# Optimization experiments

Hardware: AMD Instinct MI355X
Metric: run time of the kernel (lower is better)

Reference implementation:

```python
import jax, jax.numpy as jnp
import numpy as np
from jax import lax

B, T, D, U = 64, 512, 512, 1024


def setup_inputs() -> dict:
    key = jax.random.key(0)
    k1, k2, k3 = jax.random.split(key, 3)
    x = jax.random.normal(k1, (B, T, D), dtype=jnp.float32)
    Wx = jax.random.normal(k2, (D, 4 * U), dtype=jnp.float32) * (1.0 / np.sqrt(D))
    Wh = jax.random.normal(k3, (U, 4 * U), dtype=jnp.float32) * (1.0 / np.sqrt(U))
    # bias init: zeros(i), ones(f), zeros(c), zeros(o)
    b = jnp.concatenate([jnp.zeros((U,)), jnp.ones((U,)), jnp.zeros((2 * U,))]).astype(jnp.float32)
    return {"x": x, "Wx": Wx, "Wh": Wh, "b": b}


def reference(x, Wx, Wh, b):
    units = Wh.shape[0]
    batch = x.shape[0]
    # Precompute input projections for all timesteps: [B, T, 4U]
    xz = jnp.einsum('btd,dz->btz', x, Wx)

    def step(carry, zx_t):
        h, c = carry
        z = zx_t + h @ Wh + b            # [B, 4U]
        zi, zf, zg, zo = jnp.split(z, 4, axis=-1)
        i = jax.nn.sigmoid(zi)
        f = jax.nn.sigmoid(zf)
        c_new = f * c + i * jnp.tanh(zg)
        o = jax.nn.sigmoid(zo)
        h_new = o * jnp.tanh(c_new)
        return (h_new, c_new), None

    h0 = jnp.zeros((batch, units), dtype=x.dtype)
    c0 = jnp.zeros((batch, units), dtype=x.dtype)
    (h_last, c_last), _ = lax.scan(step, (h0, c0), jnp.swapaxes(xz, 0, 1))
    # return_sequence=False, return_states=False -> last hidden state
    return h_last
```

## Files before the change

### kernel.cpp

```cpp
#include <hip/hip_runtime.h>
#include <hip/hip_bf16.h>


#define T_STEPS 512
#define BATCH   64
#define DIM     512
#define UNITS   1024
#define ZCOLS   4096
#define MR      16

typedef float        f32x4 __attribute__((ext_vector_type(4)));
typedef unsigned int u32x4 __attribute__((ext_vector_type(4)));

__device__ __forceinline__ f32x4 mfma16x16x32_bf16(u32x4 a, u32x4 b, f32x4 c) {
    asm("v_mfma_f32_16x16x32_bf16 %0, %1, %2, %0" : "+v"(c) : "v"(a), "v"(b));
    return c;
}

__device__ __forceinline__ unsigned short f2bf(float f) {
    union { float f; unsigned u; } v; v.f = f;
    unsigned r = v.u + 0x7fffu + ((v.u >> 16) & 1u);
    return (unsigned short)(r >> 16);
}

__device__ __forceinline__ float fsigmoid(float x) { return 1.0f / (1.0f + __expf(-x)); }
__device__ __forceinline__ float ftanh(float x)    { return 1.0f - 2.0f / (__expf(2.0f * x) + 1.0f); }

__device__ __forceinline__ u32x4 pack8(const float* __restrict__ p) {
    float4 f0 = reinterpret_cast<const float4*>(p)[0];
    float4 f1 = reinterpret_cast<const float4*>(p)[1];
    u32x4 r;
    r.x = (unsigned)f2bf(f0.x) | ((unsigned)f2bf(f0.y) << 16);
    r.y = (unsigned)f2bf(f0.z) | ((unsigned)f2bf(f0.w) << 16);
    r.z = (unsigned)f2bf(f1.x) | ((unsigned)f2bf(f1.y) << 16);
    r.w = (unsigned)f2bf(f1.z) | ((unsigned)f2bf(f1.w) << 16);
    return r;
}

#define LD4(d, base) \
    asm volatile("global_load_dwordx4 %0, %1, off sc0 sc1" : "=v"(d) : "v"(base));
#define WAITV0 \
    asm volatile("s_waitcnt vmcnt(0)" ::: "memory"); \
    __builtin_amdgcn_sched_barrier(0);


__global__ void k_transpose_bf16(const float* __restrict__ in, unsigned short* __restrict__ out,
                                 int K, int N) {
    __shared__ float tile[32][33];
    int n0 = blockIdx.x * 32, k0 = blockIdx.y * 32;
    int tx = threadIdx.x, ty = threadIdx.y;
    tile[ty][tx] = in[(size_t)(k0 + ty) * N + n0 + tx];
    __syncthreads();
    out[(size_t)(n0 + ty) * K + k0 + tx] = f2bf(tile[tx][ty]);
}

__global__ void k_init(unsigned int* __restrict__ hbuf_u32, float* __restrict__ cbuf,
                       unsigned int* __restrict__ flags) {
    int i = blockIdx.x * blockDim.x + threadIdx.x;
    if (i < 65536) hbuf_u32[i] = 0u;
    else if (i < 131072) cbuf[i - 65536] = 0.0f;
    else if (i < 131072 + 4096) flags[i - 131072] = 0u;
}

__global__ __launch_bounds__(512, 2) void k_xproj(
        const float* __restrict__ x,
        const unsigned short* __restrict__ WxT,
        const float* __restrict__ bias,
        float* __restrict__ xz,
        int base) {
    const int tid  = threadIdx.x;
    const int lane = tid & 63;
    const int w    = tid >> 6;
    const int n0   = blockIdx.x * 512 + w * 64;
    const int t    = blockIdx.y;
    const int r16  = lane & 15;
    const int kl   = (lane >> 4) * 8;

    __shared__ __align__(16) unsigned short as_[64 * 512];

    for (int i = tid; i < 4096; i += 512) {
        int row = i >> 6, kc = i & 63;
        u32x4 v = pack8(x + ((size_t)row * T_STEPS + base + t) * DIM + kc * 8);
        int lb = (row * 1024 + kc * 16) ^ ((row & 7) << 4);
        *reinterpret_cast<u32x4*>(reinterpret_cast<char*>(as_) + lb) = v;
    }
    __syncthreads();

    const unsigned short* bp = WxT + (size_t)(n0 + r16) * DIM + kl;

    f32x4 acc[4][4] = {};
    asm volatile("s_nop 1" : "+v"(acc[0][0]), "+v"(acc[1][1]), "+v"(acc[2][2]), "+v"(acc[3][3]));

    #pragma unroll 2
    for (int kk = 0; kk < 16; ++kk) {
        u32x4 b0 = *reinterpret_cast<const u32x4*>(bp + kk * 32);
        u32x4 b1 = *reinterpret_cast<const u32x4*>(bp + 16 * DIM + kk * 32);
        u32x4 b2 = *reinterpret_cast<const u32x4*>(bp + 32 * DIM + kk * 32);
        u32x4 b3 = *reinterpret_cast<const u32x4*>(bp + 48 * DIM + kk * 32);
        u32x4 a[4];
        #pragma unroll
        for (int mt = 0; mt < 4; ++mt) {
            int row = mt * 16 + r16;
            int lb = (row * 1024 + (kk * 32 + kl) * 2) ^ ((row & 7) << 4);
            a[mt] = *reinterpret_cast<const u32x4*>(reinterpret_cast<const char*>(as_) + lb);
        }
        #pragma unroll
        for (int mt = 0; mt < 4; ++mt) {
            acc[mt][0] = mfma16x16x32_bf16(a[mt], b0, acc[mt][0]);
            acc[mt][1] = mfma16x16x32_bf16(a[mt], b1, acc[mt][1]);
            acc[mt][2] = mfma16x16x32_bf16(a[mt], b2, acc[mt][2]);
            acc[mt][3] = mfma16x16x32_bf16(a[mt], b3, acc[mt][3]);
        }
    }
    asm volatile("s_nop 7\n\ts_nop 7" : "+v"(acc[0][0]), "+v"(acc[1][1]), "+v"(acc[2][2]), "+v"(acc[3][3]));

    const int rowq = (lane >> 4) * 4;
    #pragma unroll
    for (int nt = 0; nt < 4; ++nt) {
        const int col = n0 + nt * 16 + r16;
        const float bv = bias[col];
        #pragma unroll
        for (int mt = 0; mt < 4; ++mt)
            #pragma unroll
            for (int r = 0; r < 4; ++r)
                xz[((size_t)t * BATCH + mt * 16 + rowq + r) * ZCOLS + col] = acc[mt][nt][r] + bv;
    }
}

__global__ __launch_bounds__(512, 1) void k_lstm(
        const float* __restrict__ xz,
        const unsigned short* __restrict__ WhT,
        unsigned short* hbuf,
        float* __restrict__ cbuf,
        float* __restrict__ out,
        unsigned int* flags,
        int base_step, int tc) {
    const int tid  = threadIdx.x;
    const int lane = tid & 63;
    const int w    = tid >> 6;
    const int ct   = w & 3;
    const int kh   = w >> 2;
    const int mg   = blockIdx.x >> 5;
    const int zb   = blockIdx.x & 31;
    const int r0   = mg * MR;
    const int u0   = zb * 32;
    const int c16  = lane & 15;
    const int klb  = (lane >> 4) * 16;

    __shared__ __align__(16) unsigned short hs[MR * 1024];
    __shared__ float zbuf[2][MR][132];

    u32x4 breg[2][16];
    #pragma unroll
    for (int n = 0; n < 2; ++n) {
        const unsigned short* wp =
            WhT + ((size_t)(ct * UNITS + u0 + n * 16 + c16)) * UNITS + kh * 512 + (lane >> 4) * 8;
        #pragma unroll
        for (int kk = 0; kk < 16; ++kk) {
            breg[n][kk] = *reinterpret_cast<const u32x4*>(wp + kk * 32);
            asm volatile("" : "+v"(breg[n][kk]));
        }
    }

    const int ri = tid >> 5;
    const int ui = tid & 31;
    float creg = cbuf[(size_t)(r0 + ri) * UNITS + u0 + ui];

    unsigned int* const myflag = flags + (size_t)blockIdx.x * 32;
    const unsigned int* const gflags = flags + (size_t)mg * 32 * 32;

    for (int t = 0; t < tc; ++t) {
        const int s = base_step + t;
        const unsigned short* hrd = hbuf + (size_t)(s & 1) * (BATCH * UNITS);

        {
            u32x4 sv[4];
            #pragma unroll
            for (int j = 0; j < 4; ++j) {
                int i = tid + j * 512;
                int row = i >> 7, kc = i & 127;
                const unsigned short* src = hrd + (size_t)(r0 + row) * UNITS + kc * 8;
                LD4(sv[j], src)
            }
            WAITV0
            #pragma unroll
            for (int j = 0; j < 4; ++j) {
                int i = tid + j * 512;
                int row = i >> 7, kc = i & 127;
                int lb = (row * 2048 + kc * 16) ^ ((row & 7) << 4);
                *reinterpret_cast<u32x4*>(reinterpret_cast<char*>(hs) + lb) = sv[j];
            }
        }
        __syncthreads();

        const float* xp = xz + ((size_t)t * BATCH + r0 + ri) * ZCOLS + u0 + ui;
        float xv0 = xp[0], xv1 = xp[UNITS], xv2 = xp[2 * UNITS], xv3 = xp[3 * UNITS];

        f32x4 acc0 = {0, 0, 0, 0}, acc1 = {0, 0, 0, 0};
        asm volatile("s_nop 1" : "+v"(acc0), "+v"(acc1));
        const char* abase = reinterpret_cast<const char*>(hs);
        const int axor = (c16 & 7) << 4;
        #pragma unroll
        for (int kk = 0; kk < 16; ++kk) {
            int lb = (c16 * 2048 + kh * 1024 + kk * 64 + klb) ^ axor;
            u32x4 a = *reinterpret_cast<const u32x4*>(abase + lb);
            acc0 = mfma16x16x32_bf16(a, breg[0][kk], acc0);
            acc1 = mfma16x16x32_bf16(a, breg[1][kk], acc1);
        }
        asm volatile("s_nop 7\n\ts_nop 7" : "+v"(acc0), "+v"(acc1));
        {
            const int rowq = (lane >> 4) * 4;
            #pragma unroll
            for (int r = 0; r < 4; ++r) {
                zbuf[kh][rowq + r][ct * 32 + c16]      = acc0[r];
                zbuf[kh][rowq + r][ct * 32 + 16 + c16] = acc1[r];
            }
        }
        __syncthreads();

        {
            float zi = zbuf[0][ri][ui]      + zbuf[1][ri][ui]      + xv0;
            float zf = zbuf[0][ri][32 + ui] + zbuf[1][ri][32 + ui] + xv1;
            float zg = zbuf[0][ri][64 + ui] + zbuf[1][ri][64 + ui] + xv2;
            float zo = zbuf[0][ri][96 + ui] + zbuf[1][ri][96 + ui] + xv3;
            float ig = fsigmoid(zi), fg = fsigmoid(zf), gg = ftanh(zg), og = fsigmoid(zo);
            creg = fg * creg + ig * gg;
            float hn = og * ftanh(creg);
            unsigned hv = f2bf(hn);
            unsigned short* hwp = hbuf + (size_t)((s + 1) & 1) * (BATCH * UNITS)
                                  + (size_t)(r0 + ri) * UNITS + u0 + ui;
            asm volatile("global_store_short %0, %1, off sc0 sc1" :: "v"(hwp), "v"(hv) : "memory");
            if (s == T_STEPS - 1) out[(size_t)(r0 + ri) * UNITS + u0 + ui] = hn;
        }

        if (t < tc - 1) {
            WAITV0
            __syncthreads();
            if (tid == 0) {
                unsigned fv = (unsigned)(s + 1);
                asm volatile("global_store_dword %0, %1, off sc0 sc1"
                             :: "v"(myflag), "v"(fv) : "memory");
                asm volatile("s_waitcnt vmcnt(0)" ::: "memory");
            }
            if (w == 0) {
                const unsigned tgt = (unsigned)(s + 1);
                const unsigned int* fp = gflags + (size_t)(lane & 31) * 32;
                int iter = 0;
                for (;;) {
                    unsigned v;
                    asm volatile("global_load_dword %0, %1, off sc0 sc1\n\ts_waitcnt vmcnt(0)"
                                 : "=v"(v) : "v"(fp) : "memory");
                    if (__all((int)(v >= tgt))) break;
                    if (++iter > (1 << 20)) break;
                    __builtin_amdgcn_s_sleep(1);
                }
            }
            __syncthreads();
        }
    }
    cbuf[(size_t)(r0 + ri) * UNITS + u0 + ui] = creg;
}


extern "C" void kernel_launch(void* const* d_in, const int* in_sizes, int n_in,
                              void* d_out, int out_size, void* d_ws, size_t ws_size,
                              hipStream_t stream) {
    const float* x    = (const float*)d_in[0];
    const float* Wx   = (const float*)d_in[1];
    const float* Wh   = (const float*)d_in[2];
    const float* bias = (const float*)d_in[3];

    char* ws = (char*)d_ws;
    unsigned short* WxT   = (unsigned short*)(ws);
    unsigned short* WhT   = (unsigned short*)(ws + (4u << 20));
    unsigned short* hbuf  = (unsigned short*)(ws + (12u << 20));
    float*          cbuf  = (float*)(ws + (12u << 20) + (256u << 10));
    unsigned int*   flags = (unsigned int*)(ws + (12u << 20) + (512u << 10));
    float*          xz    = (float*)(ws + (13u << 20));

    const size_t fixedB = 13u << 20;
    int tc = 1;
    const int cands[9] = {512, 256, 128, 64, 32, 16, 8, 4, 2};
    for (int i = 0; i < 9; ++i)
        if (fixedB + (size_t)cands[i] * (1u << 20) <= ws_size) { tc = cands[i]; break; }

    k_transpose_bf16<<<dim3(128, 16), dim3(32, 32), 0, stream>>>(Wx, WxT, 512, 4096);
    k_transpose_bf16<<<dim3(128, 32), dim3(32, 32), 0, stream>>>(Wh, WhT, 1024, 4096);
    k_init<<<512, 512, 0, stream>>>((unsigned int*)hbuf, cbuf, flags);

    const int nch = T_STEPS / tc;
    for (int ci = 0; ci < nch; ++ci) {
        k_xproj<<<dim3(8, tc), 512, 0, stream>>>(x, WxT, bias, xz, ci * tc);
        k_lstm<<<128, 512, 0, stream>>>(xz, WhT, hbuf, cbuf, (float*)d_out, flags,
                                        ci * tc, tc);
    }
}
```

Baseline: 1.905 ms.

## Replace flag barrier with step-tagged hidden-state polling and double the LSTM blocks

The per-step cross-block flag barrier is removed. Each hidden value is now stored as a 32-bit word holding the step index in its upper half and the bf16 value in its lower half, and consumers poll the h rows they need until every tag matches the current step. The LSTM grid goes from 128 to 256 blocks, with 8 batch rows per block instead of 16, so only half the threads do the elementwise gate math. This is meant to cut barrier latency and let each block wait only on the data it reads, at the cost of doubling h traffic and repeating the recurrent weight loads across more blocks. The MFMA A-tile rows beyond 8 now alias via c16&7, so half of the MFMA output is redundant.

After: 2.579 ms. 35.4% more time.

```diff
diff --git a/kernel.cpp b/kernel.cpp
--- a/kernel.cpp
+++ b/kernel.cpp
@@ -7,7 +7,6 @@
 #define DIM     512
 #define UNITS   1024
 #define ZCOLS   4096
-#define MR      16
 
 typedef float        f32x4 __attribute__((ext_vector_type(4)));
 typedef unsigned int u32x4 __attribute__((ext_vector_type(4)));
@@ -37,8 +36,8 @@
     return r;
 }
 
-#define LD4(d, base) \
-    asm volatile("global_load_dwordx4 %0, %1, off sc0 sc1" : "=v"(d) : "v"(base));
+#define LDX4T(d, p) \
+    asm volatile("global_load_dwordx4 %0, %1, off sc0 sc1" : "=v"(d) : "v"(p));
 #define WAITV0 \
     asm volatile("s_waitcnt vmcnt(0)" ::: "memory"); \
     __builtin_amdgcn_sched_barrier(0);
@@ -54,12 +53,10 @@
     out[(size_t)(n0 + ty) * K + k0 + tx] = f2bf(tile[tx][ty]);
 }
 
-__global__ void k_init(unsigned int* __restrict__ hbuf_u32, float* __restrict__ cbuf,
-                       unsigned int* __restrict__ flags) {
+__global__ void k_init(unsigned int* __restrict__ hbuf_u32, float* __restrict__ cbuf) {
     int i = blockIdx.x * blockDim.x + threadIdx.x;
-    if (i < 65536) hbuf_u32[i] = 0u;
-    else if (i < 131072) cbuf[i - 65536] = 0.0f;
-    else if (i < 131072 + 4096) flags[i - 131072] = 0u;
+    if (i < 131072) hbuf_u32[i] = 0u;
+    else if (i < 196608) cbuf[i - 131072] = 0.0f;
 }
 
 __global__ __launch_bounds__(512, 2) void k_xproj(
@@ -130,25 +127,24 @@
 __global__ __launch_bounds__(512, 1) void k_lstm(
         const float* __restrict__ xz,
         const unsigned short* __restrict__ WhT,
-        unsigned short* hbuf,
+        unsigned int* hbuf,
         float* __restrict__ cbuf,
         float* __restrict__ out,
-        unsigned int* flags,
         int base_step, int tc) {
     const int tid  = threadIdx.x;
     const int lane = tid & 63;
     const int w    = tid >> 6;
     const int ct   = w & 3;
     const int kh   = w >> 2;
-    const int mg   = blockIdx.x >> 5;
-    const int zb   = blockIdx.x & 31;
-    const int r0   = mg * MR;
-    const int u0   = zb * 32;
+    const int grp  = blockIdx.x & 7;
+    const int zs   = blockIdx.x >> 3;
+    const int r0   = grp * 8;
+    const int u0   = zs * 32;
     const int c16  = lane & 15;
     const int klb  = (lane >> 4) * 16;
 
-    __shared__ __align__(16) unsigned short hs[MR * 1024];
-    __shared__ float zbuf[2][MR][132];
+    __shared__ __align__(16) unsigned short hs[8 * 1024];
+    __shared__ float zb[32 * 132];
 
     u32x4 breg[2][16];
     #pragma unroll
@@ -164,46 +160,66 @@
 
     const int ri = tid >> 5;
     const int ui = tid & 31;
-    float creg = cbuf[(size_t)(r0 + ri) * UNITS + u0 + ui];
-
-    unsigned int* const myflag = flags + (size_t)blockIdx.x * 32;
-    const unsigned int* const gflags = flags + (size_t)mg * 32 * 32;
+    float creg = 0.0f;
+    if (tid < 256) creg = cbuf[(size_t)(r0 + ri) * UNITS + u0 + ui];
+
+    const int srow  = tid >> 6;
+    const int scol0 = (tid & 63) * 16;
+    const int sbase = srow * 2048 + scol0 * 2;
+    const int sxor  = (srow & 7) << 4;
 
     for (int t = 0; t < tc; ++t) {
         const int s = base_step + t;
-        const unsigned short* hrd = hbuf + (size_t)(s & 1) * (BATCH * UNITS);
 
         {
-            u32x4 sv[4];
-            #pragma unroll
-            for (int j = 0; j < 4; ++j) {
-                int i = tid + j * 512;
-                int row = i >> 7, kc = i & 127;
-                const unsigned short* src = hrd + (size_t)(r0 + row) * UNITS + kc * 8;
-                LD4(sv[j], src)
+            const unsigned int* sp = hbuf + (size_t)(s & 1) * (BATCH * UNITS)
+                                     + (size_t)(r0 + srow) * UNITS + scol0;
+            const unsigned want = (unsigned)s;
+            u32x4 v0, v1, v2, v3;
+            int iter = 0;
+            for (;;) {
+                LDX4T(v0, sp) LDX4T(v1, sp + 4) LDX4T(v2, sp + 8) LDX4T(v3, sp + 12)
+                WAITV0
+                bool ok = ((v0.x >> 16) == want) & ((v0.y >> 16) == want) &
+                          ((v0.z >> 16) == want) & ((v0.w >> 16) == want) &
+                          ((v1.x >> 16) == want) & ((v1.y >> 16) == want) &
+                          ((v1.z >> 16) == want) & ((v1.w >> 16) == want) &
+                          ((v2.x >> 16) == want) & ((v2.y >> 16) == want) &
+                          ((v2.z >> 16) == want) & ((v2.w >> 16) == want) &
+                          ((v3.x >> 16) == want) & ((v3.y >> 16) == want) &
+                          ((v3.z >> 16) == want) & ((v3.w >> 16) == want);
+                if (ok) break;
+                if (++iter > (1 << 16)) break;
+                __builtin_amdgcn_s_sleep(1);
             }
-            WAITV0
-            #pragma unroll
-            for (int j = 0; j < 4; ++j) {
-                int i = tid + j * 512;
-                int row = i >> 7, kc = i & 127;
-                int lb = (row * 2048 + kc * 16) ^ ((row & 7) << 4);
-                *reinterpret_cast<u32x4*>(reinterpret_cast<char*>(hs) + lb) = sv[j];
-            }
+            u32x4 A, B;
+            A.x = (v0.x & 0xffffu) | (v0.y << 16);
+            A.y = (v0.z & 0xffffu) | (v0.w << 16);
+            A.z = (v1.x & 0xffffu) | (v1.y << 16);
+            A.w = (v1.z & 0xffffu) | (v1.w << 16);
+            B.x = (v2.x & 0xffffu) | (v2.y << 16);
+            B.y = (v2.z & 0xffffu) | (v2.w << 16);
+            B.z = (v3.x & 0xffffu) | (v3.y << 16);
+            B.w = (v3.z & 0xffffu) | (v3.w << 16);
+            *reinterpret_cast<u32x4*>(reinterpret_cast<char*>(hs) + (sbase ^ sxor))        = A;
+            *reinterpret_cast<u32x4*>(reinterpret_cast<char*>(hs) + ((sbase + 16) ^ sxor)) = B;
         }
         __syncthreads();
 
-        const float* xp = xz + ((size_t)t * BATCH + r0 + ri) * ZCOLS + u0 + ui;
-        float xv0 = xp[0], xv1 = xp[UNITS], xv2 = xp[2 * UNITS], xv3 = xp[3 * UNITS];
+        float xv0 = 0, xv1 = 0, xv2 = 0, xv3 = 0;
+        if (tid < 256) {
+            const float* xp = xz + ((size_t)t * BATCH + r0 + ri) * ZCOLS + u0 + ui;
+            xv0 = xp[0]; xv1 = xp[UNITS]; xv2 = xp[2 * UNITS]; xv3 = xp[3 * UNITS];
+        }
 
         f32x4 acc0 = {0, 0, 0, 0}, acc1 = {0, 0, 0, 0};
         asm volatile("s_nop 1" : "+v"(acc0), "+v"(acc1));
         const char* abase = reinterpret_cast<const char*>(hs);
         const int axor = (c16 & 7) << 4;
+        const int aoff = (c16 & 7) * 2048 + kh * 1024 + klb;
         #pragma unroll
         for (int kk = 0; kk < 16; ++kk) {
-            int lb = (c16 * 2048 + kh * 1024 + kk * 64 + klb) ^ axor;
-            u32x4 a = *reinterpret_cast<const u32x4*>(abase + lb);
+            u32x4 a = *reinterpret_cast<const u32x4*>(abase + ((aoff + kk * 64) ^ axor));
             acc0 = mfma16x16x32_bf16(a, breg[0][kk], acc0);
             acc1 = mfma16x16x32_bf16(a, breg[1][kk], acc1);
         }
@@ -212,53 +228,28 @@
             const int rowq = (lane >> 4) * 4;
             #pragma unroll
             for (int r = 0; r < 4; ++r) {
-                zbuf[kh][rowq + r][ct * 32 + c16]      = acc0[r];
-                zbuf[kh][rowq + r][ct * 32 + 16 + c16] = acc1[r];
+                zb[(kh * 16 + rowq + r) * 132 + ct * 32 + c16]      = acc0[r];
+                zb[(kh * 16 + rowq + r) * 132 + ct * 32 + 16 + c16] = acc1[r];
             }
         }
         __syncthreads();
 
-        {
-            float zi = zbuf[0][ri][ui]      + zbuf[1][ri][ui]      + xv0;
-            float zf = zbuf[0][ri][32 + ui] + zbuf[1][ri][32 + ui] + xv1;
-            float zg = zbuf[0][ri][64 + ui] + zbuf[1][ri][64 + ui] + xv2;
-            float zo = zbuf[0][ri][96 + ui] + zbuf[1][ri][96 + ui] + xv3;
+        if (tid < 256) {
+            float zi = zb[ri * 132 + ui]      + zb[(16 + ri) * 132 + ui]      + xv0;
+            float zf = zb[ri * 132 + 32 + ui] + zb[(16 + ri) * 132 + 32 + ui] + xv1;
+            float zg = zb[ri * 132 + 64 + ui] + zb[(16 + ri) * 132 + 64 + ui] + xv2;
+            float zo = zb[ri * 132 + 96 + ui] + zb[(16 + ri) * 132 + 96 + ui] + xv3;
             float ig = fsigmoid(zi), fg = fsigmoid(zf), gg = ftanh(zg), og = fsigmoid(zo);
             creg = fg * creg + ig * gg;
             float hn = og * ftanh(creg);
-            unsigned hv = f2bf(hn);
-            unsigned short* hwp = hbuf + (size_t)((s + 1) & 1) * (BATCH * UNITS)
-                                  + (size_t)(r0 + ri) * UNITS + u0 + ui;
-            asm volatile("global_store_short %0, %1, off sc0 sc1" :: "v"(hwp), "v"(hv) : "memory");
+            unsigned hv = ((unsigned)(s + 1) << 16) | (unsigned)f2bf(hn);
+            unsigned int* hwp = hbuf + (size_t)((s + 1) & 1) * (BATCH * UNITS)
+                                + (size_t)(r0 + ri) * UNITS + u0 + ui;
+            asm volatile("global_store_dword %0, %1, off sc0 sc1" :: "v"(hwp), "v"(hv) : "memory");
             if (s == T_STEPS - 1) out[(size_t)(r0 + ri) * UNITS + u0 + ui] = hn;
         }
-
-        if (t < tc - 1) {
-            WAITV0
-            __syncthreads();
-            if (tid == 0) {
-                unsigned fv = (unsigned)(s + 1);
-                asm volatile("global_store_dword %0, %1, off sc0 sc1"
-                             :: "v"(myflag), "v"(fv) : "memory");
-                asm volatile("s_waitcnt vmcnt(0)" ::: "memory");
-            }
-            if (w == 0) {
-                const unsigned tgt = (unsigned)(s + 1);
-                const unsigned int* fp = gflags + (size_t)(lane & 31) * 32;
-                int iter = 0;
-                for (;;) {
-                    unsigned v;
-                    asm volatile("global_load_dword %0, %1, off sc0 sc1\n\ts_waitcnt vmcnt(0)"
-                                 : "=v"(v) : "v"(fp) : "memory");
-                    if (__all((int)(v >= tgt))) break;
-                    if (++iter > (1 << 20)) break;
-                    __builtin_amdgcn_s_sleep(1);
-                }
-            }
-            __syncthreads();
-        }
-    }
-    cbuf[(size_t)(r0 + ri) * UNITS + u0 + ui] = creg;
+    }
+    if (tid < 256) cbuf[(size_t)(r0 + ri) * UNITS + u0 + ui] = creg;
 }
 
 
@@ -273,9 +264,8 @@
     char* ws = (char*)d_ws;
     unsigned short* WxT   = (unsigned short*)(ws);
     unsigned short* WhT   = (unsigned short*)(ws + (4u << 20));
-    unsigned short* hbuf  = (unsigned short*)(ws + (12u << 20));
-    float*          cbuf  = (float*)(ws + (12u << 20) + (256u << 10));
-    unsigned int*   flags = (unsigned int*)(ws + (12u << 20) + (512u << 10));
+    unsigned int*   hbuf  = (unsigned int*)(ws + (12u << 20));
+    float*          cbuf  = (float*)(ws + (12u << 20) + (512u << 10));
     float*          xz    = (float*)(ws + (13u << 20));
 
     const size_t fixedB = 13u << 20;
@@ -286,12 +276,12 @@
 
     k_transpose_bf16<<<dim3(128, 16), dim3(32, 32), 0, stream>>>(Wx, WxT, 512, 4096);
     k_transpose_bf16<<<dim3(128, 32), dim3(32, 32), 0, stream>>>(Wh, WhT, 1024, 4096);
-    k_init<<<512, 512, 0, stream>>>((unsigned int*)hbuf, cbuf, flags);
+    k_init<<<512, 512, 0, stream>>>(hbuf, cbuf);
 
     const int nch = T_STEPS / tc;
     for (int ci = 0; ci < nch; ++ci) {
         k_xproj<<<dim3(8, tc), 512, 0, stream>>>(x, WxT, bias, xz, ci * tc);
-        k_lstm<<<128, 512, 0, stream>>>(xz, WhT, hbuf, cbuf, (float*)d_out, flags,
+        k_lstm<<<256, 512, 0, stream>>>(xz, WhT, hbuf, cbuf, (float*)d_out,
                                         ci * tc, tc);
     }
 }
```

## Fuse input projection into persistent LSTM kernel, compute next step during barrier wait

Applied to the files above, without the earlier changes.

Removes the separate xproj kernel and its global xz buffer. Each persistent LSTM block now computes its own slice of x_t·Wx with MFMA, using a small shared x tile and a double-buffered xzb array. The projection for step s+1 runs after the block publishes its flag and before it spins on the other blocks' flags, so the work is meant to hide inside the grid-wide sync wait. This drops the global round trip of the projection output and the chunked multi-launch structure. In exchange each step reloads Wx fragments from global or L2, and the spin-wait iteration cap is lowered.

Result: slower. 3.660 ms (+92.1%).

```diff
diff --git a/kernel.cpp b/kernel.cpp
--- a/kernel.cpp
+++ b/kernel.cpp
@@ -54,87 +54,20 @@
     out[(size_t)(n0 + ty) * K + k0 + tx] = f2bf(tile[tx][ty]);
 }
 
-__global__ void k_init(unsigned int* __restrict__ hbuf_u32, float* __restrict__ cbuf,
-                       unsigned int* __restrict__ flags) {
+__global__ void k_init(unsigned int* __restrict__ hbuf_u32, unsigned int* __restrict__ flags) {
     int i = blockIdx.x * blockDim.x + threadIdx.x;
     if (i < 65536) hbuf_u32[i] = 0u;
-    else if (i < 131072) cbuf[i - 65536] = 0.0f;
-    else if (i < 131072 + 4096) flags[i - 131072] = 0u;
-}
-
-__global__ __launch_bounds__(512, 2) void k_xproj(
+    else if (i < 65536 + 4096) flags[i - 65536] = 0u;
+}
+
+__global__ __launch_bounds__(512, 1) void k_lstm(
         const float* __restrict__ x,
         const unsigned short* __restrict__ WxT,
+        const unsigned short* __restrict__ WhT,
         const float* __restrict__ bias,
-        float* __restrict__ xz,
-        int base) {
-    const int tid  = threadIdx.x;
-    const int lane = tid & 63;
-    const int w    = tid >> 6;
-    const int n0   = blockIdx.x * 512 + w * 64;
-    const int t    = blockIdx.y;
-    const int r16  = lane & 15;
-    const int kl   = (lane >> 4) * 8;
-
-    __shared__ __align__(16) unsigned short as_[64 * 512];
-
-    for (int i = tid; i < 4096; i += 512) {
-        int row = i >> 6, kc = i & 63;
-        u32x4 v = pack8(x + ((size_t)row * T_STEPS + base + t) * DIM + kc * 8);
-        int lb = (row * 1024 + kc * 16) ^ ((row & 7) << 4);
-        *reinterpret_cast<u32x4*>(reinterpret_cast<char*>(as_) + lb) = v;
-    }
-    __syncthreads();
-
-    const unsigned short* bp = WxT + (size_t)(n0 + r16) * DIM + kl;
-
-    f32x4 acc[4][4] = {};
-    asm volatile("s_nop 1" : "+v"(acc[0][0]), "+v"(acc[1][1]), "+v"(acc[2][2]), "+v"(acc[3][3]));
-
-    #pragma unroll 2
-    for (int kk = 0; kk < 16; ++kk) {
-        u32x4 b0 = *reinterpret_cast<const u32x4*>(bp + kk * 32);
-        u32x4 b1 = *reinterpret_cast<const u32x4*>(bp + 16 * DIM + kk * 32);
-        u32x4 b2 = *reinterpret_cast<const u32x4*>(bp + 32 * DIM + kk * 32);
-        u32x4 b3 = *reinterpret_cast<const u32x4*>(bp + 48 * DIM + kk * 32);
-        u32x4 a[4];
-        #pragma unroll
-        for (int mt = 0; mt < 4; ++mt) {
-            int row = mt * 16 + r16;
-            int lb = (row * 1024 + (kk * 32 + kl) * 2) ^ ((row & 7) << 4);
-            a[mt] = *reinterpret_cast<const u32x4*>(reinterpret_cast<const char*>(as_) + lb);
-        }
-        #pragma unroll
-        for (int mt = 0; mt < 4; ++mt) {
-            acc[mt][0] = mfma16x16x32_bf16(a[mt], b0, acc[mt][0]);
-            acc[mt][1] = mfma16x16x32_bf16(a[mt], b1, acc[mt][1]);
-            acc[mt][2] = mfma16x16x32_bf16(a[mt], b2, acc[mt][2]);
-            acc[mt][3] = mfma16x16x32_bf16(a[mt], b3, acc[mt][3]);
-        }
-    }
-    asm volatile("s_nop 7\n\ts_nop 7" : "+v"(acc[0][0]), "+v"(acc[1][1]), "+v"(acc[2][2]), "+v"(acc[3][3]));
-
-    const int rowq = (lane >> 4) * 4;
-    #pragma unroll
-    for (int nt = 0; nt < 4; ++nt) {
-        const int col = n0 + nt * 16 + r16;
-        const float bv = bias[col];
-        #pragma unroll
-        for (int mt = 0; mt < 4; ++mt)
-            #pragma unroll
-            for (int r = 0; r < 4; ++r)
-                xz[((size_t)t * BATCH + mt * 16 + rowq + r) * ZCOLS + col] = acc[mt][nt][r] + bv;
-    }
-}
-
-__global__ __launch_bounds__(512, 1) void k_lstm(
-        const float* __restrict__ xz,
-        const unsigned short* __restrict__ WhT,
         unsigned short* hbuf,
-        float* __restrict__ cbuf,
         float* __restrict__ out,
-        unsigned int* flags,
-        int base_step, int tc) {
+        unsigned int* flags) {
     const int tid  = threadIdx.x;
     const int lane = tid & 63;
     const int w    = tid >> 6;
@@ -145,16 +78,19 @@
     const int r0   = mg * MR;
     const int u0   = zb * 32;
     const int c16  = lane & 15;
+    const int kl   = (lane >> 4) * 8;
     const int klb  = (lane >> 4) * 16;
 
     __shared__ __align__(16) unsigned short hs[MR * 1024];
     __shared__ float zbuf[2][MR][132];
+    __shared__ __align__(16) unsigned short xs[MR * 512];
+    __shared__ float xzb[2][MR][132];
 
     u32x4 breg[2][16];
     #pragma unroll
     for (int n = 0; n < 2; ++n) {
         const unsigned short* wp =
-            WhT + ((size_t)(ct * UNITS + u0 + n * 16 + c16)) * UNITS + kh * 512 + (lane >> 4) * 8;
+            WhT + ((size_t)(ct * UNITS + u0 + n * 16 + c16)) * UNITS + kh * 512 + kl;
         #pragma unroll
         for (int kk = 0; kk < 16; ++kk) {
             breg[n][kk] = *reinterpret_cast<const u32x4*>(wp + kk * 32);
@@ -164,13 +100,47 @@
 
     const int ri = tid >> 5;
     const int ui = tid & 31;
-    float creg = cbuf[(size_t)(r0 + ri) * UNITS + u0 + ui];
+    float creg = 0.0f;
+    float bi0 = bias[u0 + ui];
+    float bi1 = bias[UNITS + u0 + ui];
+    float bi2 = bias[2 * UNITS + u0 + ui];
+    float bi3 = bias[3 * UNITS + u0 + ui];
 
     unsigned int* const myflag = flags + (size_t)blockIdx.x * 32;
     const unsigned int* const gflags = flags + (size_t)mg * 32 * 32;
 
-    for (int t = 0; t < tc; ++t) {
-        const int s = base_step + t;
+    const unsigned short* const bpx =
+        WxT + ((size_t)((w >> 1) * UNITS + u0 + (w & 1) * 16 + c16)) * DIM + kl;
+
+
+    {
+        #pragma unroll
+        for (int j = 0; j < 2; ++j) {
+            int i = tid + j * 512;
+            int row = i >> 6, kc8 = i & 63;
+            u32x4 v = pack8(x + ((size_t)(r0 + row) * T_STEPS + 0) * DIM + kc8 * 8);
+            int lb = (row * 1024 + kc8 * 16) ^ ((row & 7) << 4);
+            *reinterpret_cast<u32x4*>(reinterpret_cast<char*>(xs) + lb) = v;
+        }
+        __syncthreads();
+        f32x4 xacc = {0, 0, 0, 0};
+        asm volatile("s_nop 1" : "+v"(xacc));
+        #pragma unroll
+        for (int kk = 0; kk < 16; ++kk) {
+            u32x4 b = *reinterpret_cast<const u32x4*>(bpx + kk * 32);
+            int lb = (c16 * 1024 + (kk * 32 + kl) * 2) ^ ((c16 & 7) << 4);
+            u32x4 a = *reinterpret_cast<const u32x4*>(reinterpret_cast<const char*>(xs) + lb);
+            xacc = mfma16x16x32_bf16(a, b, xacc);
+        }
+        asm volatile("s_nop 7\n\ts_nop 7" : "+v"(xacc));
+        const int rowq = (lane >> 4) * 4;
+        #pragma unroll
+        for (int r = 0; r < 4; ++r)
+            xzb[0][rowq + r][w * 16 + c16] = xacc[r];
+        __syncthreads();
+    }
+
+    for (int s = 0; s < T_STEPS; ++s) {
         const unsigned short* hrd = hbuf + (size_t)(s & 1) * (BATCH * UNITS);
 
         {
@@ -193,9 +163,6 @@
         }
         __syncthreads();
 
-        const float* xp = xz + ((size_t)t * BATCH + r0 + ri) * ZCOLS + u0 + ui;
-        float xv0 = xp[0], xv1 = xp[UNITS], xv2 = xp[2 * UNITS], xv3 = xp[3 * UNITS];
-
         f32x4 acc0 = {0, 0, 0, 0}, acc1 = {0, 0, 0, 0};
         asm volatile("s_nop 1" : "+v"(acc0), "+v"(acc1));
         const char* abase = reinterpret_cast<const char*>(hs);
@@ -219,10 +186,11 @@
         __syncthreads();
 
         {
-            float zi = zbuf[0][ri][ui]      + zbuf[1][ri][ui]      + xv0;
-            float zf = zbuf[0][ri][32 + ui] + zbuf[1][ri][32 + ui] + xv1;
-            float zg = zbuf[0][ri][64 + ui] + zbuf[1][ri][64 + ui] + xv2;
-            float zo = zbuf[0][ri][96 + ui] + zbuf[1][ri][96 + ui] + xv3;
+            const float* xzr = xzb[s & 1][ri];
+            float zi = zbuf[0][ri][ui]      + zbuf[1][ri][ui]      + xzr[ui]      + bi0;
+            float zf = zbuf[0][ri][32 + ui] + zbuf[1][ri][32 + ui] + xzr[32 + ui] + bi1;
+            float zg = zbuf[0][ri][64 + ui] + zbuf[1][ri][64 + ui] + xzr[64 + ui] + bi2;
+            float zo = zbuf[0][ri][96 + ui] + zbuf[1][ri][96 + ui] + xzr[96 + ui] + bi3;
             float ig = fsigmoid(zi), fg = fsigmoid(zf), gg = ftanh(zg), og = fsigmoid(zo);
             creg = fg * creg + ig * gg;
             float hn = og * ftanh(creg);
@@ -233,7 +201,7 @@
             if (s == T_STEPS - 1) out[(size_t)(r0 + ri) * UNITS + u0 + ui] = hn;
         }
 
-        if (t < tc - 1) {
+        if (s < T_STEPS - 1) {
             WAITV0
             __syncthreads();
             if (tid == 0) {
@@ -242,6 +210,34 @@
                              :: "v"(myflag), "v"(fv) : "memory");
                 asm volatile("s_waitcnt vmcnt(0)" ::: "memory");
             }
+
+            {
+                #pragma unroll
+                for (int j = 0; j < 2; ++j) {
+                    int i = tid + j * 512;
+                    int row = i >> 6, kc8 = i & 63;
+                    u32x4 v = pack8(x + ((size_t)(r0 + row) * T_STEPS + (s + 1)) * DIM + kc8 * 8);
+                    int lb = (row * 1024 + kc8 * 16) ^ ((row & 7) << 4);
+                    *reinterpret_cast<u32x4*>(reinterpret_cast<char*>(xs) + lb) = v;
+                }
+                __syncthreads();
+                f32x4 xacc = {0, 0, 0, 0};
+                asm volatile("s_nop 1" : "+v"(xacc));
+                #pragma unroll
+                for (int kk = 0; kk < 16; ++kk) {
+                    u32x4 b = *reinterpret_cast<const u32x4*>(bpx + kk * 32);
+                    int lb = (c16 * 1024 + (kk * 32 + kl) * 2) ^ ((c16 & 7) << 4);
+                    u32x4 a = *reinterpret_cast<const u32x4*>(reinterpret_cast<const char*>(xs) + lb);
+                    xacc = mfma16x16x32_bf16(a, b, xacc);
+                }
+                asm volatile("s_nop 7\n\ts_nop 7" : "+v"(xacc));
+                const int rowq = (lane >> 4) * 4;
+                #pragma unroll
+                for (int r = 0; r < 4; ++r)
+                    xzb[(s + 1) & 1][rowq + r][w * 16 + c16] = xacc[r];
+            }
+            __syncthreads();
+
             if (w == 0) {
                 const unsigned tgt = (unsigned)(s + 1);
                 const unsigned int* fp = gflags + (size_t)(lane & 31) * 32;
@@ -251,14 +247,13 @@
                     asm volatile("global_load_dword %0, %1, off sc0 sc1\n\ts_waitcnt vmcnt(0)"
                                  : "=v"(v) : "v"(fp) : "memory");
                     if (__all((int)(v >= tgt))) break;
-                    if (++iter > (1 << 20)) break;
+                    if (++iter > (1 << 18)) break;
                     __builtin_amdgcn_s_sleep(1);
                 }
             }
             __syncthreads();
         }
     }
-    cbuf[(size_t)(r0 + ri) * UNITS + u0 + ui] = creg;
 }
 
 
@@ -274,24 +269,11 @@
     unsigned short* WxT   = (unsigned short*)(ws);
     unsigned short* WhT   = (unsigned short*)(ws + (4u << 20));
     unsigned short* hbuf  = (unsigned short*)(ws + (12u << 20));
-    float*          cbuf  = (float*)(ws + (12u << 20) + (256u << 10));
-    unsigned int*   flags = (unsigned int*)(ws + (12u << 20) + (512u << 10));
-    float*          xz    = (float*)(ws + (13u << 20));
-
-    const size_t fixedB = 13u << 20;
-    int tc = 1;
-    const int cands[9] = {512, 256, 128, 64, 32, 16, 8, 4, 2};
-    for (int i = 0; i < 9; ++i)
-        if (fixedB + (size_t)cands[i] * (1u << 20) <= ws_size) { tc = cands[i]; break; }
+    unsigned int*   flags = (unsigned int*)(ws + (12u << 20) + (256u << 10));
 
     k_transpose_bf16<<<dim3(128, 16), dim3(32, 32), 0, stream>>>(Wx, WxT, 512, 4096);
     k_transpose_bf16<<<dim3(128, 32), dim3(32, 32), 0, stream>>>(Wh, WhT, 1024, 4096);
-    k_init<<<512, 512, 0, stream>>>((unsigned int*)hbuf, cbuf, flags);
-
-    const int nch = T_STEPS / tc;
-    for (int ci = 0; ci < nch; ++ci) {
-        k_xproj<<<dim3(8, tc), 512, 0, stream>>>(x, WxT, bias, xz, ci * tc);
-        k_lstm<<<128, 512, 0, stream>>>(xz, WhT, hbuf, cbuf, (float*)d_out, flags,
-                                        ci * tc, tc);
-    }
-}
+    k_init<<<160, 512, 0, stream>>>((unsigned int*)hbuf, flags);
+
+    k_lstm<<<128, 512, 0, stream>>>(x, WxT, WhT, bias, hbuf, (float*)d_out, flags);
+}
```

## Fuse input projection and LSTM recurrence into one persistent producer-consumer kernel

Applied to the files above, without the earlier changes.

Replaces the separate x-projection and recurrent kernels with a single persistent kernel of 256 blocks. 128 blocks run the recurrence and 128 producer blocks compute the input projection into a 64-step ring buffer, coordinated through global flags. This overlaps the input GEMM with the serial recurrence and avoids materializing the full xz tensor and the chunked launches. It relies on all 256 blocks being co-resident and adds spin-wait overhead in the recurrence loop, which now also polls the xz flags each step.

After: 1.643 ms, median of 2. 13.8% less time.

```diff
diff --git a/kernel.cpp b/kernel.cpp
--- a/kernel.cpp
+++ b/kernel.cpp
@@ -8,6 +8,7 @@
 #define UNITS   1024
 #define ZCOLS   4096
 #define MR      16
+#define RING    64
 
 typedef float        f32x4 __attribute__((ext_vector_type(4)));
 typedef unsigned int u32x4 __attribute__((ext_vector_type(4)));
@@ -39,6 +40,11 @@
 
 #define LD4(d, base) \
     asm volatile("global_load_dwordx4 %0, %1, off sc0 sc1" : "=v"(d) : "v"(base));
+#define LDW(d, base) \
+    asm volatile("global_load_dword %0, %1, off sc0 sc1\n\ts_waitcnt vmcnt(0)" \
+                 : "=v"(d) : "v"(base) : "memory");
+#define STW(base, v) \
+    asm volatile("global_store_dword %0, %1, off sc0 sc1" :: "v"(base), "v"(v) : "memory");
 #define WAITV0 \
     asm volatile("s_waitcnt vmcnt(0)" ::: "memory"); \
     __builtin_amdgcn_sched_barrier(0);
@@ -54,211 +60,259 @@
     out[(size_t)(n0 + ty) * K + k0 + tx] = f2bf(tile[tx][ty]);
 }
 
-__global__ void k_init(unsigned int* __restrict__ hbuf_u32, float* __restrict__ cbuf,
-                       unsigned int* __restrict__ flags) {
+__global__ void k_init(unsigned int* __restrict__ hbuf_u32,
+                       unsigned int* __restrict__ hflags,
+                       unsigned int* __restrict__ xzflags) {
     int i = blockIdx.x * blockDim.x + threadIdx.x;
     if (i < 65536) hbuf_u32[i] = 0u;
-    else if (i < 131072) cbuf[i - 65536] = 0.0f;
-    else if (i < 131072 + 4096) flags[i - 131072] = 0u;
-}
-
-__global__ __launch_bounds__(512, 2) void k_xproj(
+    else if (i < 65536 + 4096) hflags[i - 65536] = 0u;
+    else if (i < 65536 + 4096 + 512) xzflags[i - 69632] = 0u;
+}
+
+__global__ __launch_bounds__(512, 1) void k_fused(
         const float* __restrict__ x,
         const unsigned short* __restrict__ WxT,
+        const unsigned short* __restrict__ WhT,
         const float* __restrict__ bias,
-        float* __restrict__ xz,
-        int base) {
+        unsigned short* hbuf,
+        float* __restrict__ out,
+        unsigned int* hflags,
+        unsigned int* xzflags,
+        float* __restrict__ xzring) {
+    __shared__ __align__(16) char smem[65536];
     const int tid  = threadIdx.x;
     const int lane = tid & 63;
     const int w    = tid >> 6;
-    const int n0   = blockIdx.x * 512 + w * 64;
-    const int t    = blockIdx.y;
-    const int r16  = lane & 15;
-    const int kl   = (lane >> 4) * 8;
-
-    __shared__ __align__(16) unsigned short as_[64 * 512];
-
-    for (int i = tid; i < 4096; i += 512) {
-        int row = i >> 6, kc = i & 63;
-        u32x4 v = pack8(x + ((size_t)row * T_STEPS + base + t) * DIM + kc * 8);
-        int lb = (row * 1024 + kc * 16) ^ ((row & 7) << 4);
-        *reinterpret_cast<u32x4*>(reinterpret_cast<char*>(as_) + lb) = v;
-    }
-    __syncthreads();
-
-    const unsigned short* bp = WxT + (size_t)(n0 + r16) * DIM + kl;
-
-    f32x4 acc[4][4] = {};
-    asm volatile("s_nop 1" : "+v"(acc[0][0]), "+v"(acc[1][1]), "+v"(acc[2][2]), "+v"(acc[3][3]));
-
-    #pragma unroll 2
-    for (int kk = 0; kk < 16; ++kk) {
-        u32x4 b0 = *reinterpret_cast<const u32x4*>(bp + kk * 32);
-        u32x4 b1 = *reinterpret_cast<const u32x4*>(bp + 16 * DIM + kk * 32);
-        u32x4 b2 = *reinterpret_cast<const u32x4*>(bp + 32 * DIM + kk * 32);
-        u32x4 b3 = *reinterpret_cast<const u32x4*>(bp + 48 * DIM + kk * 32);
-        u32x4 a[4];
+
+    if (blockIdx.x < 128) {
+        unsigned short* hs = (unsigned short*)smem;
+        float* zb = (float*)(smem + 32768);
+        const int ct  = w & 3;
+        const int kh  = w >> 2;
+        const int mg  = blockIdx.x >> 5;
+        const int zbk = blockIdx.x & 31;
+        const int r0  = mg * MR;
+        const int u0  = zbk * 32;
+        const int c16 = lane & 15;
+        const int kl  = (lane >> 4) * 8;
+        const int klb = (lane >> 4) * 16;
+
+        u32x4 breg[2][16];
         #pragma unroll
-        for (int mt = 0; mt < 4; ++mt) {
-            int row = mt * 16 + r16;
-            int lb = (row * 1024 + (kk * 32 + kl) * 2) ^ ((row & 7) << 4);
-            a[mt] = *reinterpret_cast<const u32x4*>(reinterpret_cast<const char*>(as_) + lb);
+        for (int n = 0; n < 2; ++n) {
+            const unsigned short* wp =
+                WhT + ((size_t)(ct * UNITS + u0 + n * 16 + c16)) * UNITS + kh * 512 + kl;
+            #pragma unroll
+            for (int kk = 0; kk < 16; ++kk) {
+                breg[n][kk] = *reinterpret_cast<const u32x4*>(wp + kk * 32);
+                asm volatile("" : "+v"(breg[n][kk]));
+            }
         }
-        #pragma unroll
-        for (int mt = 0; mt < 4; ++mt) {
-            acc[mt][0] = mfma16x16x32_bf16(a[mt], b0, acc[mt][0]);
-            acc[mt][1] = mfma16x16x32_bf16(a[mt], b1, acc[mt][1]);
-            acc[mt][2] = mfma16x16x32_bf16(a[mt], b2, acc[mt][2]);
-            acc[mt][3] = mfma16x16x32_bf16(a[mt], b3, acc[mt][3]);
+
+        const int ri = tid >> 5;
+        const int ui = tid & 31;
+        float creg = 0.0f;
+
+        unsigned int* const myflag = hflags + (size_t)blockIdx.x * 32;
+        const unsigned int* const gflags = hflags + (size_t)mg * 32 * 32;
+
+        if (w == 0) {
+            const unsigned int* fp = xzflags + (lane & 7);
+            int iter = 0;
+            for (;;) {
+                unsigned v; LDW(v, fp)
+                bool ok = (lane < 8) ? (v == 1u) : true;
+                if (__all((int)ok)) break;
+                if (++iter > (1 << 20)) break;
+                __builtin_amdgcn_s_sleep(1);
+            }
+        }
+        __syncthreads();
+
+        for (int s = 0; s < T_STEPS; ++s) {
+            const unsigned short* hrd = hbuf + (size_t)(s & 1) * (BATCH * UNITS);
+
+            {
+                u32x4 sv[4];
+                #pragma unroll
+                for (int j = 0; j < 4; ++j) {
+                    int i = tid + j * 512;
+                    int row = i >> 7, kc = i & 127;
+                    const unsigned short* src = hrd + (size_t)(r0 + row) * UNITS + kc * 8;
+                    LD4(sv[j], src)
+                }
+                WAITV0
+                #pragma unroll
+                for (int j = 0; j < 4; ++j) {
+                    int i = tid + j * 512;
+                    int row = i >> 7, kc = i & 127;
+                    int lb = (row * 2048 + kc * 16) ^ ((row & 7) << 4);
+                    *reinterpret_cast<u32x4*>(reinterpret_cast<char*>(hs) + lb) = sv[j];
+                }
+            }
+            __syncthreads();
+
+            float xv0, xv1, xv2, xv3;
+            {
+                const float* xp = xzring + ((size_t)(s & (RING - 1)) * BATCH + r0 + ri) * ZCOLS
+                                  + u0 + ui;
+                asm volatile("global_load_dword %0, %1, off sc0 sc1" : "=v"(xv0) : "v"(xp));
+                asm volatile("global_load_dword %0, %1, off sc0 sc1" : "=v"(xv1) : "v"(xp + UNITS));
+                asm volatile("global_load_dword %0, %1, off sc0 sc1" : "=v"(xv2) : "v"(xp + 2 * UNITS));
+                asm volatile("global_load_dword %0, %1, off sc0 sc1" : "=v"(xv3) : "v"(xp + 3 * UNITS));
+            }
+
+            f32x4 acc0 = {0, 0, 0, 0}, acc1 = {0, 0, 0, 0};
+            asm volatile("s_nop 1" : "+v"(acc0), "+v"(acc1));
+            const char* abase = reinterpret_cast<const char*>(hs);
+            const int axor = (c16 & 7) << 4;
+            #pragma unroll
+            for (int kk = 0; kk < 16; ++kk) {
+                int lb = (c16 * 2048 + kh * 1024 + kk * 64 + klb) ^ axor;
+                u32x4 a = *reinterpret_cast<const u32x4*>(abase + lb);
+                acc0 = mfma16x16x32_bf16(a, breg[0][kk], acc0);
+                acc1 = mfma16x16x32_bf16(a, breg[1][kk], acc1);
+            }
+            asm volatile("s_nop 7\n\ts_nop 7" : "+v"(acc0), "+v"(acc1));
+            {
+                const int rowq = (lane >> 4) * 4;
+                #pragma unroll
+                for (int r = 0; r < 4; ++r) {
+                    zb[((kh * 16 + rowq + r)) * 132 + ct * 32 + c16]      = acc0[r];
+                    zb[((kh * 16 + rowq + r)) * 132 + ct * 32 + 16 + c16] = acc1[r];
+                }
+            }
+            __syncthreads();
+            WAITV0
+
+            {
+                float zi = zb[ri * 132 + ui]      + zb[(16 + ri) * 132 + ui]      + xv0;
+                float zf = zb[ri * 132 + 32 + ui] + zb[(16 + ri) * 132 + 32 + ui] + xv1;
+                float zg = zb[ri * 132 + 64 + ui] + zb[(16 + ri) * 132 + 64 + ui] + xv2;
+                float zo = zb[ri * 132 + 96 + ui] + zb[(16 + ri) * 132 + 96 + ui] + xv3;
+                float ig = fsigmoid(zi), fg = fsigmoid(zf), gg = ftanh(zg), og = fsigmoid(zo);
+                creg = fg * creg + ig * gg;
+                float hn = og * ftanh(creg);
+                unsigned hv = f2bf(hn);
+                unsigned short* hwp = hbuf + (size_t)((s + 1) & 1) * (BATCH * UNITS)
+                                      + (size_t)(r0 + ri) * UNITS + u0 + ui;
+                asm volatile("global_store_short %0, %1, off sc0 sc1" :: "v"(hwp), "v"(hv) : "memory");
+                if (s == T_STEPS - 1) out[(size_t)(r0 + ri) * UNITS + u0 + ui] = hn;
+            }
+
+            if (s < T_STEPS - 1) {
+                WAITV0
+                __syncthreads();
+                if (tid == 0) {
+                    STW(myflag, (unsigned)(s + 1))
+                    asm volatile("s_waitcnt vmcnt(0)" ::: "memory");
+                }
+                if (w == 0) {
+                    const unsigned tgtH = (unsigned)(s + 1);
+                    const unsigned tgtX = (unsigned)(s + 2);
+                    const unsigned int* fp = (lane < 32)
+                        ? gflags + (size_t)lane * 32
+                        : xzflags + (size_t)((s + 1) & (RING - 1)) * 8 + (lane & 7);
+                    int iter = 0;
+                    for (;;) {
+                        unsigned v; LDW(v, fp)
+                        bool ok = (lane < 32) ? (v >= tgtH)
+                                  : ((lane < 40) ? (v == tgtX) : true);
+                        if (__all((int)ok)) break;
+                        if (++iter > (1 << 20)) break;
+                        __builtin_amdgcn_s_sleep(1);
+                    }
+                }
+                __syncthreads();
+            }
+        }
+    } else {
+        unsigned short* as_ = (unsigned short*)smem;
+        const int p   = blockIdx.x - 128;
+        const int bx  = p & 7;
+        const int jt  = p >> 3;
+        const int n0  = bx * 512 + w * 64;
+        const int r16 = lane & 15;
+        const int kl  = (lane >> 4) * 8;
+
+        for (int k2 = 0; k2 < T_STEPS / 16; ++k2) {
+            const int t = jt + 16 * k2;
+
+            if (t >= RING) {
+                if (w == 0) {
+                    const unsigned need = (unsigned)(t - RING + 1);
+                    int iter = 0;
+                    for (;;) {
+                        unsigned v0, v1;
+                        LDW(v0, hflags + (size_t)lane * 32)
+                        LDW(v1, hflags + (size_t)(lane + 64) * 32)
+                        if (__all((int)(v0 >= need && v1 >= need))) break;
+                        if (++iter > (1 << 20)) break;
+                        __builtin_amdgcn_s_sleep(1);
+                    }
+                }
+                __syncthreads();
+            }
+
+            for (int i = tid; i < 4096; i += 512) {
+                int row = i >> 6, kc8 = i & 63;
+                u32x4 v = pack8(x + ((size_t)row * T_STEPS + t) * DIM + kc8 * 8);
+                int lb = (row * 1024 + kc8 * 16) ^ ((row & 7) << 4);
+                *reinterpret_cast<u32x4*>(reinterpret_cast<char*>(as_) + lb) = v;
+            }
+            __syncthreads();
+
+            const unsigned short* bp = WxT + (size_t)(n0 + r16) * DIM + kl;
+            f32x4 acc[4][4] = {};
+            asm volatile("s_nop 1" : "+v"(acc[0][0]), "+v"(acc[1][1]), "+v"(acc[2][2]), "+v"(acc[3][3]));
+            #pragma unroll 2
+            for (int kk = 0; kk < 16; ++kk) {
+                u32x4 b0 = *reinterpret_cast<const u32x4*>(bp + kk * 32);
+                u32x4 b1 = *reinterpret_cast<const u32x4*>(bp + 16 * DIM + kk * 32);
+                u32x4 b2 = *reinterpret_cast<const u32x4*>(bp + 32 * DIM + kk * 32);
+                u32x4 b3 = *reinterpret_cast<const u32x4*>(bp + 48 * DIM + kk * 32);
+                u32x4 a[4];
+                #pragma unroll
+                for (int mt = 0; mt < 4; ++mt) {
+                    int row = mt * 16 + r16;
+                    int lb = (row * 1024 + (kk * 32 + kl) * 2) ^ ((row & 7) << 4);
+                    a[mt] = *reinterpret_cast<const u32x4*>(reinterpret_cast<const char*>(as_) + lb);
+                }
+                #pragma unroll
+                for (int mt = 0; mt < 4; ++mt) {
+                    acc[mt][0] = mfma16x16x32_bf16(a[mt], b0, acc[mt][0]);
+                    acc[mt][1] = mfma16x16x32_bf16(a[mt], b1, acc[mt][1]);
+                    acc[mt][2] = mfma16x16x32_bf16(a[mt], b2, acc[mt][2]);
+                    acc[mt][3] = mfma16x16x32_bf16(a[mt], b3, acc[mt][3]);
+                }
+            }
+            asm volatile("s_nop 7\n\ts_nop 7" : "+v"(acc[0][0]), "+v"(acc[1][1]), "+v"(acc[2][2]), "+v"(acc[3][3]));
+
+            {
+                float* ringb = xzring + (size_t)(t & (RING - 1)) * BATCH * ZCOLS;
+                const int rowq = (lane >> 4) * 4;
+                #pragma unroll
+                for (int nt = 0; nt < 4; ++nt) {
+                    const int col = n0 + nt * 16 + r16;
+                    const float bv = bias[col];
+                    #pragma unroll
+                    for (int mt = 0; mt < 4; ++mt) {
+                        #pragma unroll
+                        for (int r = 0; r < 4; ++r) {
+                            float val = acc[mt][nt][r] + bv;
+                            float* dst = ringb + (size_t)(mt * 16 + rowq + r) * ZCOLS + col;
+                            asm volatile("global_store_dword %0, %1, off sc0 sc1"
+                                         :: "v"(dst), "v"(val) : "memory");
+                        }
+                    }
+                }
+            }
+            WAITV0
+            __syncthreads();
+            if (tid == 0) STW(xzflags + (size_t)(t & (RING - 1)) * 8 + bx, (unsigned)(t + 1))
+            __syncthreads();
         }
     }
-    asm volatile("s_nop 7\n\ts_nop 7" : "+v"(acc[0][0]), "+v"(acc[1][1]), "+v"(acc[2][2]), "+v"(acc[3][3]));
-
-    const int rowq = (lane >> 4) * 4;
-    #pragma unroll
-    for (int nt = 0; nt < 4; ++nt) {
-        const int col = n0 + nt * 16 + r16;
-        const float bv = bias[col];
-        #pragma unroll
-        for (int mt = 0; mt < 4; ++mt)
-            #pragma unroll
-            for (int r = 0; r < 4; ++r)
-                xz[((size_t)t * BATCH + mt * 16 + rowq + r) * ZCOLS + col] = acc[mt][nt][r] + bv;
-    }
-}
-
-__global__ __launch_bounds__(512, 1) void k_lstm(
-        const float* __restrict__ xz,
-        const unsigned short* __restrict__ WhT,
-        unsigned short* hbuf,
-        float* __restrict__ cbuf,
-        float* __restrict__ out,
-        unsigned int* flags,
-        int base_step, int tc) {
-    const int tid  = threadIdx.x;
-    const int lane = tid & 63;
-    const int w    = tid >> 6;
-    const int ct   = w & 3;
-    const int kh   = w >> 2;
-    const int mg   = blockIdx.x >> 5;
-    const int zb   = blockIdx.x & 31;
-    const int r0   = mg * MR;
-    const int u0   = zb * 32;
-    const int c16  = lane & 15;
-    const int klb  = (lane >> 4) * 16;
-
-    __shared__ __align__(16) unsigned short hs[MR * 1024];
-    __shared__ float zbuf[2][MR][132];
-
-    u32x4 breg[2][16];
-    #pragma unroll
-    for (int n = 0; n < 2; ++n) {
-        const unsigned short* wp =
-            WhT + ((size_t)(ct * UNITS + u0 + n * 16 + c16)) * UNITS + kh * 512 + (lane >> 4) * 8;
-        #pragma unroll
-        for (int kk = 0; kk < 16; ++kk) {
-            breg[n][kk] = *reinterpret_cast<const u32x4*>(wp + kk * 32);
-            asm volatile("" : "+v"(breg[n][kk]));
-        }
-    }
-
-    const int ri = tid >> 5;
-    const int ui = tid & 31;
-    float creg = cbuf[(size_t)(r0 + ri) * UNITS + u0 + ui];
-
-    unsigned int* const myflag = flags + (size_t)blockIdx.x * 32;
-    const unsigned int* const gflags = flags + (size_t)mg * 32 * 32;
-
-    for (int t = 0; t < tc; ++t) {
-        const int s = base_step + t;
-        const unsigned short* hrd = hbuf + (size_t)(s & 1) * (BATCH * UNITS);
-
-        {
-            u32x4 sv[4];
-            #pragma unroll
-            for (int j = 0; j < 4; ++j) {
-                int i = tid + j * 512;
-                int row = i >> 7, kc = i & 127;
-                const unsigned short* src = hrd + (size_t)(r0 + row) * UNITS + kc * 8;
-                LD4(sv[j], src)
-            }
-            WAITV0
-            #pragma unroll
-            for (int j = 0; j < 4; ++j) {
-                int i = tid + j * 512;
-                int row = i >> 7, kc = i & 127;
-                int lb = (row * 2048 + kc * 16) ^ ((row & 7) << 4);
-                *reinterpret_cast<u32x4*>(reinterpret_cast<char*>(hs) + lb) = sv[j];
-            }
-        }
-        __syncthreads();
-
-        const float* xp = xz + ((size_t)t * BATCH + r0 + ri) * ZCOLS + u0 + ui;
-        float xv0 = xp[0], xv1 = xp[UNITS], xv2 = xp[2 * UNITS], xv3 = xp[3 * UNITS];
-
-        f32x4 acc0 = {0, 0, 0, 0}, acc1 = {0, 0, 0, 0};
-        asm volatile("s_nop 1" : "+v"(acc0), "+v"(acc1));
-        const char* abase = reinterpret_cast<const char*>(hs);
-        const int axor = (c16 & 7) << 4;
-        #pragma unroll
-        for (int kk = 0; kk < 16; ++kk) {
-            int lb = (c16 * 2048 + kh * 1024 + kk * 64 + klb) ^ axor;
-            u32x4 a = *reinterpret_cast<const u32x4*>(abase + lb);
-            acc0 = mfma16x16x32_bf16(a, breg[0][kk], acc0);
-            acc1 = mfma16x16x32_bf16(a, breg[1][kk], acc1);
-        }
-        asm volatile("s_nop 7\n\ts_nop 7" : "+v"(acc0), "+v"(acc1));
-        {
-            const int rowq = (lane >> 4) * 4;
-            #pragma unroll
-            for (int r = 0; r < 4; ++r) {
-                zbuf[kh][rowq + r][ct * 32 + c16]      = acc0[r];
-                zbuf[kh][rowq + r][ct * 32 + 16 + c16] = acc1[r];
-            }
-        }
-        __syncthreads();
-
-        {
-            float zi = zbuf[0][ri][ui]      + zbuf[1][ri][ui]      + xv0;
-            float zf = zbuf[0][ri][32 + ui] + zbuf[1][ri][32 + ui] + xv1;
-            float zg = zbuf[0][ri][64 + ui] + zbuf[1][ri][64 + ui] + xv2;
-            float zo = zbuf[0][ri][96 + ui] + zbuf[1][ri][96 + ui] + xv3;
-            float ig = fsigmoid(zi), fg = fsigmoid(zf), gg = ftanh(zg), og = fsigmoid(zo);
-            creg = fg * creg + ig * gg;
-            float hn = og * ftanh(creg);
-            unsigned hv = f2bf(hn);
-            unsigned short* hwp = hbuf + (size_t)((s + 1) & 1) * (BATCH * UNITS)
-                                  + (size_t)(r0 + ri) * UNITS + u0 + ui;
-            asm volatile("global_store_short %0, %1, off sc0 sc1" :: "v"(hwp), "v"(hv) : "memory");
-            if (s == T_STEPS - 1) out[(size_t)(r0 + ri) * UNITS + u0 + ui] = hn;
-        }
-
-        if (t < tc - 1) {
-            WAITV0
-            __syncthreads();
-            if (tid == 0) {
-                unsigned fv = (unsigned)(s + 1);
-                asm volatile("global_store_dword %0, %1, off sc0 sc1"
-                             :: "v"(myflag), "v"(fv) : "memory");
-                asm volatile("s_waitcnt vmcnt(0)" ::: "memory");
-            }
-            if (w == 0) {
-                const unsigned tgt = (unsigned)(s + 1);
-                const unsigned int* fp = gflags + (size_t)(lane & 31) * 32;
-                int iter = 0;
-                for (;;) {
-                    unsigned v;
-                    asm volatile("global_load_dword %0, %1, off sc0 sc1\n\ts_waitcnt vmcnt(0)"
-                                 : "=v"(v) : "v"(fp) : "memory");
-                    if (__all((int)(v >= tgt))) break;
-                    if (++iter > (1 << 20)) break;
-                    __builtin_amdgcn_s_sleep(1);
-                }
-            }
-            __syncthreads();
-        }
-    }
-    cbuf[(size_t)(r0 + ri) * UNITS + u0 + ui] = creg;
 }
 
 
@@ -271,27 +325,17 @@
     const float* bias = (const float*)d_in[3];
 
     char* ws = (char*)d_ws;
-    unsigned short* WxT   = (unsigned short*)(ws);
-    unsigned short* WhT   = (unsigned short*)(ws + (4u << 20));
-    unsigned short* hbuf  = (unsigned short*)(ws + (12u << 20));
-    float*          cbuf  = (float*)(ws + (12u << 20) + (256u << 10));
-    unsigned int*   flags = (unsigned int*)(ws + (12u << 20) + (512u << 10));
-    float*          xz    = (float*)(ws + (13u << 20));
-
-    const size_t fixedB = 13u << 20;
-    int tc = 1;
-    const int cands[9] = {512, 256, 128, 64, 32, 16, 8, 4, 2};
-    for (int i = 0; i < 9; ++i)
-        if (fixedB + (size_t)cands[i] * (1u << 20) <= ws_size) { tc = cands[i]; break; }
+    unsigned short* WxT     = (unsigned short*)(ws);
+    unsigned short* WhT     = (unsigned short*)(ws + (4u << 20));
+    unsigned short* hbuf    = (unsigned short*)(ws + (12u << 20));
+    unsigned int*   hflags  = (unsigned int*)(ws + (12u << 20) + (256u << 10));
+    unsigned int*   xzflags = (unsigned int*)(ws + (12u << 20) + (272u << 10));
+    float*          xzring  = (float*)(ws + (13u << 20));
 
     k_transpose_bf16<<<dim3(128, 16), dim3(32, 32), 0, stream>>>(Wx, WxT, 512, 4096);
     k_transpose_bf16<<<dim3(128, 32), dim3(32, 32), 0, stream>>>(Wh, WhT, 1024, 4096);
-    k_init<<<512, 512, 0, stream>>>((unsigned int*)hbuf, cbuf, flags);
-
-    const int nch = T_STEPS / tc;
-    for (int ci = 0; ci < nch; ++ci) {
-        k_xproj<<<dim3(8, tc), 512, 0, stream>>>(x, WxT, bias, xz, ci * tc);
-        k_lstm<<<128, 512, 0, stream>>>(xz, WhT, hbuf, cbuf, (float*)d_out, flags,
-                                        ci * tc, tc);
-    }
-}
+    k_init<<<160, 512, 0, stream>>>((unsigned int*)hbuf, hflags, xzflags);
+
+    k_fused<<<256, 512, 0, stream>>>(x, WxT, WhT, bias, hbuf, (float*)d_out,
+                                     hflags, xzflags, xzring);
+}
```
